# Optimization experiments

Measured on AMD Instinct MI355X. Metric: run time of the kernel, lower is better.

The kernel has to match this reference:

```python
import jax, jax.numpy as jnp
import numpy as np

B, T, D, H, OUT, VOCAB = 64, 100, 1024, 1024, 28, 28


def setup_inputs() -> dict:
    key = jax.random.key(0)
    ks = jax.random.split(key, 12)
    s = 0.05
    return {
        "x": jax.random.normal(ks[0], (B, T, D), jnp.float32),
        # encoder GRU (keras reset_after=True): kernel [D,3H], recurrent [H,3H], bias [2,3H]
        "enc_W": jax.random.normal(ks[1], (D, 3 * H), jnp.float32) * s,
        "enc_U": jax.random.normal(ks[2], (H, 3 * H), jnp.float32) * s,
        "enc_b": jax.random.normal(ks[3], (2, 3 * H), jnp.float32) * s,
        # AdditiveAttention learned scale vector [H]
        "att_scale": jax.random.normal(ks[4], (H,), jnp.float32) * s,
        # Embedding(28, H)
        "emb_W": jax.random.normal(ks[5], (VOCAB, H), jnp.float32) * s,
        # decoder GRUCell
        "dec_W": jax.random.normal(ks[6], (H, 3 * H), jnp.float32) * s,
        "dec_U": jax.random.normal(ks[7], (H, 3 * H), jnp.float32) * s,
        "dec_b": jax.random.normal(ks[8], (2, 3 * H), jnp.float32) * s,
        # fc: Dense(OUT) on concat([h, context]) -> [2H, OUT]
        "fc_W": jax.random.normal(ks[9], (2 * H, OUT), jnp.float32) * s,
        "fc_b": jax.random.normal(ks[10], (OUT,), jnp.float32) * s,
    }


def _gru_update(x_t, h, W, U, b):
    # keras GRU math with reset_after=True
    mx = x_t @ W + b[0]          # [B,3H]
    mi = h @ U + b[1]            # [B,3H]
    xz, xr, xh = jnp.split(mx, 3, axis=-1)
    rz, rr, rh = jnp.split(mi, 3, axis=-1)
    z = jax.nn.sigmoid(xz + rz)
    r = jax.nn.sigmoid(xr + rr)
    hh = jnp.tanh(xh + r * rh)
    return z * h + (1.0 - z) * hh


def reference(x, enc_W, enc_U, enc_b, att_scale, emb_W, dec_W, dec_U, dec_b, fc_W, fc_b):
    b, t, _ = x.shape
    h = jnp.zeros((b, enc_U.shape[0]), x.dtype)

    # encoder GRU, return_sequences=True
    def enc_step(h, x_t):
        h = _gru_update(x_t, h, enc_W, enc_U, enc_b)
        return h, h

    _, hpe = jax.lax.scan(enc_step, h, jnp.swapaxes(x, 0, 1))  # [T,B,H]
    hpe = jnp.swapaxes(hpe, 0, 1)                              # [B,T,H]

    out_dim = fc_b.shape[0]
    p0 = jnp.zeros((b, out_dim), x.dtype)
    h0 = jnp.zeros((b, dec_U.shape[0]), x.dtype)

    def dec_step(carry, _):
        p, hd = carry
        # additive attention: scores[b,j] = sum_d scale[d]*tanh(q[b,d]+k[b,j,d])
        scores = jnp.einsum('bth,h->bt', jnp.tanh(hd[:, None, :] + hpe), att_scale)
        attn = jax.nn.softmax(scores, axis=-1)
        ctx = jnp.einsum('bt,bth->bh', attn, hpe)
        idx = jnp.argmax(p, axis=-1)          # [B] int
        e = emb_W[idx]                        # [B,H]
        hd = _gru_update(e, hd, dec_W, dec_U, dec_b)
        p = jnp.concatenate([hd, ctx], axis=1) @ fc_W + fc_b
        return (p, hd), p

    _, outs = jax.lax.scan(dec_step, (p0, h0), None, length=t)  # [T,B,OUT]
    return jnp.swapaxes(outs, 0, 1)                              # [B,T,OUT]
```

## Files before the change

kernel.cpp:

```cpp
#include <hip/hip_runtime.h>

#define TT 100
#define HH 1024
#define H3 3072
#define NOUT 28

#define AGENT __HIP_MEMORY_SCOPE_AGENT
#define WGRP  __HIP_MEMORY_SCOPE_WORKGROUP
#define SPIN_CAP (1u<<27)

__device__ __forceinline__ float frcp_(float x){ return __builtin_amdgcn_rcpf(x); }
__device__ __forceinline__ float fsig_(float x){ return frcp_(1.0f + __expf(-x)); }
__device__ __forceinline__ float ftanh_(float x){ return 1.0f - 2.0f*frcp_(__expf(2.0f*x) + 1.0f); }

__device__ __forceinline__ unsigned long long aload8(const unsigned long long* p){
    return __hip_atomic_load(p, __ATOMIC_RELAXED, AGENT);
}
__device__ __forceinline__ unsigned aload4(const int* p){
    return (unsigned)__hip_atomic_load(p, __ATOMIC_RELAXED, AGENT);
}

__device__ __forceinline__ void gridbar(int* slot, int sub, int target){
    __syncthreads();
    if (threadIdx.x == 0){
        __hip_atomic_fetch_add(slot + sub*16, 1, __ATOMIC_RELAXED, AGENT);
        unsigned gy = 0; int s;
        do {
            s = 0;
            #pragma unroll
            for (int c=0;c<16;c++) s += __hip_atomic_load(slot + c*16, __ATOMIC_RELAXED, AGENT);
            if (s < target){ if (++gy > SPIN_CAP) break; __builtin_amdgcn_s_sleep(1); }
        } while (s < target);
    }
    __syncthreads();
}

__device__ __forceinline__ void wbar4(int* c, int tgt){
    asm volatile("s_waitcnt lgkmcnt(0)" ::: "memory");
    if ((threadIdx.x & 63) == 0) __hip_atomic_fetch_add(c, 1, __ATOMIC_RELAXED, WGRP);
    unsigned gy = 0;
    while (__hip_atomic_load(c, __ATOMIC_RELAXED, WGRP) < tgt){ if (++gy > SPIN_CAP) break; }
    asm volatile("" ::: "memory");
}

__global__ void k_init(int* ib, int n){
    int g = blockIdx.x*256 + threadIdx.x;
    if (g < n) ib[g] = 0;
}

__global__ __launch_bounds__(256) void k_transpose(const float* __restrict__ U0,
                                                   const float* __restrict__ U1,
                                                   float* __restrict__ T0,
                                                   float* __restrict__ T1){
    const float* U = blockIdx.z ? U1 : U0;
    float*       T = blockIdx.z ? T1 : T0;
    __shared__ float tile[32][33];
    int tx = threadIdx.x & 31, ty = threadIdx.x >> 5;
    int j0 = blockIdx.x*32, k0 = blockIdx.y*32;
    #pragma unroll
    for (int q=0;q<4;q++){
        int kr = ty + q*8;
        tile[kr][tx] = U[(size_t)(k0+kr)*H3 + j0 + tx];
    }
    __syncthreads();
    #pragma unroll
    for (int q=0;q<4;q++){
        int jr = ty + q*8;
        T[(size_t)(j0+jr)*HH + k0 + tx] = tile[tx][jr];
    }
}

__global__ __launch_bounds__(256) void k_edec(const float* __restrict__ emb,
                                              const float* __restrict__ W,
                                              const float* __restrict__ b0,
                                              float* __restrict__ E){
    int gid = blockIdx.x*256 + threadIdx.x;
    int v = gid / H3, j = gid - v*H3;
    float acc = b0[j];
    const float* er = emb + (size_t)v*HH;
    #pragma unroll 4
    for (int k=0;k<HH;k++) acc = fmaf(er[k], W[(size_t)k*H3 + j], acc);
    E[gid] = acc;
}

__global__ __launch_bounds__(256) void k_mxgemm(const float* __restrict__ A,
                                                const float* __restrict__ W,
                                                const float* __restrict__ b0,
                                                float* __restrict__ MXT){
    __shared__ float aT[32*68];
    __shared__ float bL[32*68];
    int tid = threadIdx.x;
    int row0 = blockIdx.y*64, col0 = blockIdx.x*64;
    int arow = tid>>2, acs = (tid&3)*4;
    int bk   = tid>>3, bcs = (tid&7)*4;
    int ty = tid>>4, tx = tid&15;
    float acc[4][4] = {};
    for (int kk=0; kk<HH; kk+=32){
        #pragma unroll
        for (int i=0;i<2;i++){
            int c = acs + i*16;
            float4 v = *(const float4*)(A + (size_t)(row0+arow)*HH + kk + c);
            aT[(c+0)*68 + arow] = v.x; aT[(c+1)*68 + arow] = v.y;
            aT[(c+2)*68 + arow] = v.z; aT[(c+3)*68 + arow] = v.w;
        }
        #pragma unroll
        for (int i=0;i<2;i++){
            int c = bcs + i*32;
            float4 v = *(const float4*)(W + (size_t)(kk+bk)*H3 + col0 + c);
            *(float4*)(bL + bk*68 + c) = v;
        }
        __syncthreads();
        #pragma unroll
        for (int k=0;k<32;k++){
            float4 a4 = *(const float4*)(aT + k*68 + ty*4);
            float4 b4 = *(const float4*)(bL + k*68 + tx*4);
            acc[0][0]=fmaf(a4.x,b4.x,acc[0][0]); acc[0][1]=fmaf(a4.x,b4.y,acc[0][1]);
            acc[0][2]=fmaf(a4.x,b4.z,acc[0][2]); acc[0][3]=fmaf(a4.x,b4.w,acc[0][3]);
            acc[1][0]=fmaf(a4.y,b4.x,acc[1][0]); acc[1][1]=fmaf(a4.y,b4.y,acc[1][1]);
            acc[1][2]=fmaf(a4.y,b4.z,acc[1][2]); acc[1][3]=fmaf(a4.y,b4.w,acc[1][3]);
            acc[2][0]=fmaf(a4.z,b4.x,acc[2][0]); acc[2][1]=fmaf(a4.z,b4.y,acc[2][1]);
            acc[2][2]=fmaf(a4.z,b4.z,acc[2][2]); acc[2][3]=fmaf(a4.z,b4.w,acc[2][3]);
            acc[3][0]=fmaf(a4.w,b4.x,acc[3][0]); acc[3][1]=fmaf(a4.w,b4.y,acc[3][1]);
            acc[3][2]=fmaf(a4.w,b4.z,acc[3][2]); acc[3][3]=fmaf(a4.w,b4.w,acc[3][3]);
        }
        __syncthreads();
    }
    float4 bb = *(const float4*)(b0 + col0 + tx*4);
    #pragma unroll
    for (int i=0;i<4;i++){
        int r = row0 + ty*4 + i;
        int bq = r / 100; int tq = r - bq*100;
        float v0 = acc[i][0] + bb.x, v1 = acc[i][1] + bb.y;
        float v2 = acc[i][2] + bb.z, v3 = acc[i][3] + bb.w;
        float* dst = MXT + ((size_t)tq*H3 + col0 + tx*4)*64 + bq;
        dst[0]   = v0; dst[64]  = v1; dst[128] = v2; dst[192] = v3;
    }
}

__global__ __launch_bounds__(256) void k_enc(const float* __restrict__ MXT,
                                             const float* __restrict__ Ut,
                                             const float* __restrict__ b1,
                                             float* __restrict__ hpe,
                                             float* __restrict__ hT,
                                             int* __restrict__ bar){
    __shared__ float hs[2][16384];
    int tid = threadIdx.x, lane = tid & 63;
    int wg = blockIdx.x;
    int sub = wg & 15;
    int cu = __builtin_amdgcn_readfirstlane(wg*4 + (tid>>6));
    const float* Uz = Ut + (size_t)cu*HH;
    const float* Ur = Uz + (size_t)HH*HH;
    const float* Uh = Ur + (size_t)HH*HH;
    float bz = b1[cu], br = b1[cu+HH], bh = b1[cu+2*HH];
    for (int t=0; t<TT; ++t){
        int cur = t & 1;
        const float* mx = MXT + (size_t)t*H3*64;
        float xz = mx[(size_t)cu*64 + lane];
        float xr = mx[(size_t)(cu+HH)*64 + lane];
        float xh = mx[(size_t)(cu+2*HH)*64 + lane];
        float az=0.f, ar=0.f, ah=0.f, hp=0.f;
        if (t > 0){
            const unsigned long long* g8 = (const unsigned long long*)(hT + (size_t)cur*65536);
            unsigned long long sv[32];
            #pragma unroll
            for (int s=0;s<32;s++) sv[s] = aload8(g8 + s*256 + tid);
            #pragma unroll
            for (int s=0;s<32;s++) ((unsigned long long*)hs[0])[s*256 + tid] = sv[s];
            __syncthreads();
            for (int q=0;q<4;++q){
                if (q<3){
                    #pragma unroll
                    for (int s=0;s<32;s++) sv[s] = aload8(g8 + (q+1)*8192 + s*256 + tid);
                }
                const float* hb = hs[q&1];
                const float* Uzq = Uz + q*256;
                const float* Urq = Ur + q*256;
                const float* Uhq = Uh + q*256;
                #pragma unroll 8
                for (int k=0;k<256;++k){
                    float h = hb[k*64 + lane];
                    az = fmaf(h, Uzq[k], az);
                    ar = fmaf(h, Urq[k], ar);
                    ah = fmaf(h, Uhq[k], ah);
                }
                if ((cu>>8) == q) hp = hb[(cu&255)*64 + lane];
                if (q<3){
                    #pragma unroll
                    for (int s=0;s<32;s++) ((unsigned long long*)hs[(q+1)&1])[s*256 + tid] = sv[s];
                }
                __syncthreads();
            }
        }
        float z  = fsig_(xz + az + bz);
        float r  = fsig_(xr + ar + br);
        float hh = ftanh_(xh + r*(ah + bh));
        float hnew = z*hp + (1.f - z)*hh;
        __hip_atomic_store(hT + (size_t)(cur^1)*65536 + cu*64 + lane, hnew, __ATOMIC_RELAXED, AGENT);
        hpe[((size_t)lane*TT + t)*HH + cu] = hnew;
        gridbar(bar + (size_t)t*256, sub, 256);
    }
}

__global__ __launch_bounds__(512) void k_dec(const float* __restrict__ hpe,
                                             const float* __restrict__ Ut,
                                             const float* __restrict__ b1,
                                             const float* __restrict__ Edec,
                                             const float* __restrict__ scale,
                                             const float* __restrict__ fcW,
                                             const float* __restrict__ fcb,
                                             float* __restrict__ hdT,
                                             float* __restrict__ hdl,
                                             float* __restrict__ out,
                                             int* __restrict__ idx_t,
                                             int* __restrict__ bar,
                                             int* __restrict__ flagidx){
    __shared__ float hs[2][16384];
    __shared__ float ctxs[4][1024];
    __shared__ float s_l[128], s_e[128], m_s[4], S_s[4];
    __shared__ int c_a, c_b, c_fc, go, cstg;
    int tid = threadIdx.x, wg = blockIdx.x;
    if (tid == 0){ c_a=0; c_b=0; c_fc=0; go=0; cstg=0; }
    __syncthreads();

    if (tid < 256){
        int lane = tid & 63;
        int sub = wg & 15;
        int cu = __builtin_amdgcn_readfirstlane(wg*4 + (tid>>6));
        const float* Uz = Ut + (size_t)cu*HH;
        const float* Ur = Uz + (size_t)HH*HH;
        const float* Uh = Ur + (size_t)HH*HH;
        float bz = b1[cu], br = b1[cu+HH], bh = b1[cu+2*HH];
        int stgt = 0;
        for (int i=0; i<TT; ++i){
            int cur = i & 1;
            float az=0.f, ar=0.f, ah=0.f, hp=0.f;
            if (i > 0){
                const unsigned long long* g8 = (const unsigned long long*)(hdT + (size_t)cur*65536);
                unsigned long long sv[32];
                #pragma unroll
                for (int s=0;s<32;s++) sv[s] = aload8(g8 + s*256 + tid);
                #pragma unroll
                for (int s=0;s<32;s++) ((unsigned long long*)hs[0])[s*256 + tid] = sv[s];
                wbar4(&cstg, stgt += 4);
                for (int q=0;q<4;++q){
                    if (q<3){
                        #pragma unroll
                        for (int s=0;s<32;s++) sv[s] = aload8(g8 + (q+1)*8192 + s*256 + tid);
                    }
                    const float* hb = hs[q&1];
                    const float* Uzq = Uz + q*256;
                    const float* Urq = Ur + q*256;
                    const float* Uhq = Uh + q*256;
                    #pragma unroll 8
                    for (int k=0;k<256;++k){
                        float h = hb[k*64 + lane];
                        az = fmaf(h, Uzq[k], az);
                        ar = fmaf(h, Urq[k], ar);
                        ah = fmaf(h, Uhq[k], ah);
                    }
                    if ((cu>>8) == q) hp = hb[(cu&255)*64 + lane];
                    if (q<3){
                        #pragma unroll
                        for (int s=0;s<32;s++) ((unsigned long long*)hs[(q+1)&1])[s*256 + tid] = sv[s];
                    }
                    wbar4(&cstg, stgt += 4);
                }
            }
            if (tid == 0){
                unsigned gy = 0; int s;
                do {
                    s = 0;
                    #pragma unroll
                    for (int c=0;c<8;c++) s += __hip_atomic_load(flagidx + (size_t)i*128 + c*16, __ATOMIC_RELAXED, AGENT);
                    if (s < 64){ if (++gy > SPIN_CAP) break; __builtin_amdgcn_s_sleep(1); }
                } while (s < 64);
                __hip_atomic_store(&go, i+1, __ATOMIC_RELAXED, WGRP);
            }
            { unsigned gy=0; while (__hip_atomic_load(&go, __ATOMIC_RELAXED, WGRP) < i+1){ if (++gy > SPIN_CAP) break; } }
            asm volatile("" ::: "memory");
            unsigned mi = aload4(idx_t + (size_t)i*64 + lane);
            if (mi > 27u) mi = 0;
            const float* ed = Edec + (size_t)mi*H3;
            float xz = ed[cu], xr = ed[cu+HH], xh = ed[cu+2*HH];
            float z  = fsig_(xz + az + bz);
            float r  = fsig_(xr + ar + br);
            float hh = ftanh_(xh + r*(ah + bh));
            float hnew = z*hp + (1.f - z)*hh;
            __hip_atomic_store(hdT + (size_t)(cur^1)*65536 + cu*64 + lane, hnew, __ATOMIC_RELAXED, AGENT);
            __hip_atomic_store(hdl + (size_t)(cur^1)*65536 + (size_t)lane*HH + cu, hnew, __ATOMIC_RELAXED, AGENT);
            gridbar(bar + (size_t)i*256, sub, 256);
        }
    } else if (wg < 64){
        int t2 = tid - 256;
        int w = t2 >> 6, lane = t2 & 63, b = wg;
        float sc[16];
        #pragma unroll
        for (int s4=0;s4<4;s4++){
            float4 v = *(const float4*)(scale + lane*16 + s4*4);
            sc[s4*4+0]=v.x; sc[s4*4+1]=v.y; sc[s4*4+2]=v.z; sc[s4*4+3]=v.w;
        }
        int j0 = w*25;
        for (int i=0; i<TT; ++i){
            float q[16];
            if (i == 0){
                #pragma unroll
                for (int d=0;d<16;d++) q[d]=0.f;
            } else {
                const unsigned long long* hq8 = (const unsigned long long*)(hdl + (size_t)(i&1)*65536 + (size_t)b*HH) + lane*8;
                #pragma unroll
                for (int s8=0;s8<8;s8++){
                    unsigned long long v = aload8(hq8 + s8);
                    q[2*s8+0] = __uint_as_float((unsigned)v);
                    q[2*s8+1] = __uint_as_float((unsigned)(v>>32));
                }
            }
            if (w == 0){
                if (i > 0){
                    float acc[NOUT];
                    #pragma unroll
                    for (int o=0;o<NOUT;o++) acc[o]=0.f;
                    float cv[16];
                    #pragma unroll
                    for (int s4=0;s4<4;s4++){
                        float4 c0 = ((const float4*)ctxs[0])[lane*4+s4];
                        float4 c1 = ((const float4*)ctxs[1])[lane*4+s4];
                        float4 c2 = ((const float4*)ctxs[2])[lane*4+s4];
                        float4 c3 = ((const float4*)ctxs[3])[lane*4+s4];
                        cv[s4*4+0]=c0.x+c1.x+c2.x+c3.x;
                        cv[s4*4+1]=c0.y+c1.y+c2.y+c3.y;
                        cv[s4*4+2]=c0.z+c1.z+c2.z+c3.z;
                        cv[s4*4+3]=c0.w+c1.w+c2.w+c3.w;
                    }
                    #pragma unroll
                    for (int dd=0;dd<16;++dd){
                        int d = lane*16 + dd;
                        const float* w0p = fcW + (size_t)d*NOUT;
                        const float* w1p = fcW + (size_t)(d+HH)*NOUT;
                        float hv=q[dd], cvv=cv[dd];
                        #pragma unroll
                        for (int o=0;o<NOUT;o++) acc[o] = fmaf(hv, w0p[o], fmaf(cvv, w1p[o], acc[o]));
                    }
                    #pragma unroll
                    for (int o=0;o<NOUT;o++){
                        #pragma unroll
                        for (int m=1;m<64;m<<=1) acc[o] += __shfl_xor(acc[o], m);
                    }
                    float bv=-3.0e38f; int bi=0;
                    #pragma unroll
                    for (int o=0;o<NOUT;o++){
                        float p = acc[o] + fcb[o];
                        acc[o] = p;
                        if (p > bv){ bv = p; bi = o; }
                    }
                    float vout = 0.f;
                    #pragma unroll
                    for (int o=0;o<NOUT;o++) if (lane == o) vout = acc[o];
                    if (lane < NOUT) out[((size_t)b*TT + (i-1))*NOUT + lane] = vout;
                    if (lane == 0){
                        __hip_atomic_store(idx_t + (size_t)i*64 + b, bi, __ATOMIC_RELAXED, AGENT);
                        asm volatile("s_waitcnt vmcnt(0)" ::: "memory");
                    }
                }
                if (lane == 0){
                    __hip_atomic_fetch_add(flagidx + (size_t)i*128 + (b&7)*16, 1, __ATOMIC_RELAXED, AGENT);
                    __hip_atomic_fetch_add(&c_fc, 1, __ATOMIC_RELAXED, WGRP);
                }
            }
            float mw = -3.0e38f;
            for (int jj=0;jj<25;jj++){
                int j = j0 + jj;
                const float* hpj = hpe + ((size_t)b*TT + j)*HH + lane*16;
                float s = 0.f;
                #pragma unroll
                for (int s4=0;s4<4;s4++){
                    float4 v = *(const float4*)(hpj + s4*4);
                    s += sc[s4*4+0]*ftanh_(q[s4*4+0] + v.x);
                    s += sc[s4*4+1]*ftanh_(q[s4*4+1] + v.y);
                    s += sc[s4*4+2]*ftanh_(q[s4*4+2] + v.z);
                    s += sc[s4*4+3]*ftanh_(q[s4*4+3] + v.w);
                }
                #pragma unroll
                for (int m=1;m<64;m<<=1) s += __shfl_xor(s, m);
                if (lane == 0) s_l[j] = s;
                mw = fmaxf(mw, s);
            }
            if (lane == 0) m_s[w] = mw;
            asm volatile("s_waitcnt lgkmcnt(0)" ::: "memory");
            if (lane == 0) __hip_atomic_fetch_add(&c_a, 1, __ATOMIC_RELAXED, WGRP);
            { unsigned gy=0; while (__hip_atomic_load(&c_a, __ATOMIC_RELAXED, WGRP) < 4*(i+1)){ if (++gy > SPIN_CAP) break; } }
            asm volatile("" ::: "memory");
            float M = fmaxf(fmaxf(m_s[0],m_s[1]), fmaxf(m_s[2],m_s[3]));
            float e = 0.f;
            if (lane < 25){ e = __expf(s_l[j0+lane] - M); s_e[j0+lane] = e; }
            float Sw = e;
            #pragma unroll
            for (int m=1;m<64;m<<=1) Sw += __shfl_xor(Sw, m);
            if (lane == 0) S_s[w] = Sw;
            asm volatile("s_waitcnt lgkmcnt(0)" ::: "memory");
            if (lane == 0) __hip_atomic_fetch_add(&c_b, 1, __ATOMIC_RELAXED, WGRP);
            { unsigned gy=0; while (__hip_atomic_load(&c_b, __ATOMIC_RELAXED, WGRP) < 4*(i+1)){ if (++gy > SPIN_CAP) break; } }
            asm volatile("" ::: "memory");
            float rinv = frcp_(S_s[0]+S_s[1]+S_s[2]+S_s[3]);
            { unsigned gy=0; while (__hip_atomic_load(&c_fc, __ATOMIC_RELAXED, WGRP) < i+1){ if (++gy > SPIN_CAP) break; } }
            asm volatile("" ::: "memory");
            float a[16];
            #pragma unroll
            for (int s4=0;s4<16;s4++) a[s4]=0.f;
            for (int jj=0;jj<25;jj++){
                int j = j0 + jj;
                float wgt = s_e[j];
                const float* hpj = hpe + ((size_t)b*TT + j)*HH + lane*16;
                #pragma unroll
                for (int s4=0;s4<4;s4++){
                    float4 v = *(const float4*)(hpj + s4*4);
                    a[s4*4+0] = fmaf(wgt, v.x, a[s4*4+0]);
                    a[s4*4+1] = fmaf(wgt, v.y, a[s4*4+1]);
                    a[s4*4+2] = fmaf(wgt, v.z, a[s4*4+2]);
                    a[s4*4+3] = fmaf(wgt, v.w, a[s4*4+3]);
                }
            }
            #pragma unroll
            for (int s4=0;s4<4;s4++){
                float4 o4;
                o4.x=a[s4*4+0]*rinv; o4.y=a[s4*4+1]*rinv;
                o4.z=a[s4*4+2]*rinv; o4.w=a[s4*4+3]*rinv;
                ((float4*)ctxs[w])[lane*4 + s4] = o4;
            }
            gridbar(bar + (size_t)i*256, wg & 15, 256);
        }
        if (w == 0){
            const unsigned long long* hq8 = (const unsigned long long*)(hdl + (size_t)b*HH) + lane*8;
            float q[16];
            #pragma unroll
            for (int s8=0;s8<8;s8++){
                unsigned long long v = aload8(hq8 + s8);
                q[2*s8+0] = __uint_as_float((unsigned)v);
                q[2*s8+1] = __uint_as_float((unsigned)(v>>32));
            }
            float acc[NOUT];
            #pragma unroll
            for (int o=0;o<NOUT;o++) acc[o]=0.f;
            float cv[16];
            #pragma unroll
            for (int s4=0;s4<4;s4++){
                float4 c0 = ((const float4*)ctxs[0])[lane*4+s4];
                float4 c1 = ((const float4*)ctxs[1])[lane*4+s4];
                float4 c2 = ((const float4*)ctxs[2])[lane*4+s4];
                float4 c3 = ((const float4*)ctxs[3])[lane*4+s4];
                cv[s4*4+0]=c0.x+c1.x+c2.x+c3.x;
                cv[s4*4+1]=c0.y+c1.y+c2.y+c3.y;
                cv[s4*4+2]=c0.z+c1.z+c2.z+c3.z;
                cv[s4*4+3]=c0.w+c1.w+c2.w+c3.w;
            }
            #pragma unroll
            for (int dd=0;dd<16;++dd){
                int d = lane*16 + dd;
                const float* w0p = fcW + (size_t)d*NOUT;
                const float* w1p = fcW + (size_t)(d+HH)*NOUT;
                float hv=q[dd], cvv=cv[dd];
                #pragma unroll
                for (int o=0;o<NOUT;o++) acc[o] = fmaf(hv, w0p[o], fmaf(cvv, w1p[o], acc[o]));
            }
            #pragma unroll
            for (int o=0;o<NOUT;o++){
                #pragma unroll
                for (int m=1;m<64;m<<=1) acc[o] += __shfl_xor(acc[o], m);
            }
            float vout = 0.f;
            #pragma unroll
            for (int o=0;o<NOUT;o++) if (lane == o) vout = acc[o] + fcb[o];
            if (lane < NOUT) out[((size_t)b*TT + 99)*NOUT + lane] = vout;
        }
    } else {
        for (int i=0;i<TT;++i) gridbar(bar + (size_t)i*256, wg & 15, 256);
    }
}

extern "C" void kernel_launch(void* const* d_in, const int* in_sizes, int n_in,
                              void* d_out, int out_size, void* d_ws, size_t ws_size,
                              hipStream_t stream){
    (void)in_sizes; (void)n_in; (void)out_size; (void)ws_size;
    const float* x     = (const float*)d_in[0];
    const float* encW  = (const float*)d_in[1];
    const float* encU  = (const float*)d_in[2];
    const float* encb  = (const float*)d_in[3];
    const float* scale = (const float*)d_in[4];
    const float* emb   = (const float*)d_in[5];
    const float* decW  = (const float*)d_in[6];
    const float* decU  = (const float*)d_in[7];
    const float* decb  = (const float*)d_in[8];
    const float* fcW   = (const float*)d_in[9];
    const float* fcb   = (const float*)d_in[10];
    float* out = (float*)d_out;
    float* ws  = (float*)d_ws;

    float* MXT   = ws;
    float* encUt = MXT   + 19660800;
    float* decUt = encUt + 3145728;
    float* hpe   = decUt + 3145728;
    float* Edec  = hpe   + 6553600;
    float* hT    = Edec  + 86016;
    float* hdT   = hT    + 131072;
    float* hdl   = hdT   + 131072;
    int*   ib    = (int*)(hdl + 131072);
    int*   bar_enc = ib;
    int*   bar_dec = ib + 25600;
    int*   flagidx = ib + 51200;
    int*   idx_t   = ib + 64000;

    const float* encb1 = encb + H3;
    const float* decb1 = decb + H3;

    k_init<<<276,256,0,stream>>>(ib, 70400);
    k_transpose<<<dim3(96,32,2),256,0,stream>>>(encU, decU, encUt, decUt);
    k_edec<<<336,256,0,stream>>>(emb, decW, decb, Edec);
    k_mxgemm<<<dim3(48,100),256,0,stream>>>(x, encW, encb, MXT);
    k_enc<<<256,256,0,stream>>>(MXT, encUt, encb1, hpe, hT, bar_enc);
    k_dec<<<256,512,0,stream>>>(hpe, decUt, decb1, Edec, scale, fcW, fcb,
                                hdT, hdl, out, idx_t, bar_dec, flagidx);
}
```

Measured before the change: 11.06 ms.

## Fuse attention scores, softmax and context into single online-softmax pass

The decoder attention now computes scores, a running max/sum and the weighted context accumulation in one pass over hpe per wave, using online-softmax rescaling. This removes the second read of hpe and one intra-workgroup sync stage. The four wave partials are merged by rescaling against the global max. It also lowers the spin cap and aliases the decoder state buffers onto the dead MXT workspace. The cost is extra exp and rescale multiplies per timestep.

```diff
diff --git a/kernel.cpp b/kernel.cpp
--- a/kernel.cpp
+++ b/kernel.cpp
@@ -7,7 +7,7 @@
 
 #define AGENT __HIP_MEMORY_SCOPE_AGENT
 #define WGRP  __HIP_MEMORY_SCOPE_WORKGROUP
-#define SPIN_CAP (1u<<27)
+#define SPIN_CAP (1u<<20)
 
 __device__ __forceinline__ float frcp_(float x){ return __builtin_amdgcn_rcpf(x); }
 __device__ __forceinline__ float fsig_(float x){ return frcp_(1.0f + __expf(-x)); }
@@ -216,10 +216,10 @@
                                              int* __restrict__ flagidx){
     __shared__ float hs[2][16384];
     __shared__ float ctxs[4][1024];
-    __shared__ float s_l[128], s_e[128], m_s[4], S_s[4];
-    __shared__ int c_a, c_b, c_fc, go, cstg;
+    __shared__ float m_s[4], S_s[4];
+    __shared__ int c_a, c_fc, go, cstg;
     int tid = threadIdx.x, wg = blockIdx.x;
-    if (tid == 0){ c_a=0; c_b=0; c_fc=0; go=0; cstg=0; }
+    if (tid == 0){ c_a=0; c_fc=0; go=0; cstg=0; }
     __syncthreads();
 
     if (tid < 256){
@@ -366,64 +366,53 @@
                     __hip_atomic_fetch_add(&c_fc, 1, __ATOMIC_RELAXED, WGRP);
                 }
             }
-            float mw = -3.0e38f;
+            float m = -3.0e38f, S = 0.f;
+            float a[16];
+            #pragma unroll
+            for (int d=0;d<16;d++) a[d]=0.f;
             for (int jj=0;jj<25;jj++){
                 int j = j0 + jj;
                 const float* hpj = hpe + ((size_t)b*TT + j)*HH + lane*16;
+                float va[16];
+                {
+                    float4 v0 = *(const float4*)(hpj);
+                    float4 v1 = *(const float4*)(hpj+4);
+                    float4 v2 = *(const float4*)(hpj+8);
+                    float4 v3 = *(const float4*)(hpj+12);
+                    va[0]=v0.x;va[1]=v0.y;va[2]=v0.z;va[3]=v0.w;
+                    va[4]=v1.x;va[5]=v1.y;va[6]=v1.z;va[7]=v1.w;
+                    va[8]=v2.x;va[9]=v2.y;va[10]=v2.z;va[11]=v2.w;
+                    va[12]=v3.x;va[13]=v3.y;va[14]=v3.z;va[15]=v3.w;
+                }
                 float s = 0.f;
                 #pragma unroll
-                for (int s4=0;s4<4;s4++){
-                    float4 v = *(const float4*)(hpj + s4*4);
-                    s += sc[s4*4+0]*ftanh_(q[s4*4+0] + v.x);
-                    s += sc[s4*4+1]*ftanh_(q[s4*4+1] + v.y);
-                    s += sc[s4*4+2]*ftanh_(q[s4*4+2] + v.z);
-                    s += sc[s4*4+3]*ftanh_(q[s4*4+3] + v.w);
-                }
-                #pragma unroll
-                for (int m=1;m<64;m<<=1) s += __shfl_xor(s, m);
-                if (lane == 0) s_l[j] = s;
-                mw = fmaxf(mw, s);
-            }
-            if (lane == 0) m_s[w] = mw;
+                for (int d=0;d<16;d++) s += sc[d]*ftanh_(q[d] + va[d]);
+                #pragma unroll
+                for (int mm=1;mm<64;mm<<=1) s += __shfl_xor(s, mm);
+                float mn = fmaxf(m, s);
+                float fold = __expf(m - mn);
+                float e = __expf(s - mn);
+                S = S*fold + e;
+                #pragma unroll
+                for (int d=0;d<16;d++) a[d] = a[d]*fold + e*va[d];
+                m = mn;
+            }
+            if (lane == 0){ m_s[w] = m; S_s[w] = S; }
             asm volatile("s_waitcnt lgkmcnt(0)" ::: "memory");
             if (lane == 0) __hip_atomic_fetch_add(&c_a, 1, __ATOMIC_RELAXED, WGRP);
             { unsigned gy=0; while (__hip_atomic_load(&c_a, __ATOMIC_RELAXED, WGRP) < 4*(i+1)){ if (++gy > SPIN_CAP) break; } }
             asm volatile("" ::: "memory");
             float M = fmaxf(fmaxf(m_s[0],m_s[1]), fmaxf(m_s[2],m_s[3]));
-            float e = 0.f;
-            if (lane < 25){ e = __expf(s_l[j0+lane] - M); s_e[j0+lane] = e; }
-            float Sw = e;
-            #pragma unroll
-            for (int m=1;m<64;m<<=1) Sw += __shfl_xor(Sw, m);
-            if (lane == 0) S_s[w] = Sw;
-            asm volatile("s_waitcnt lgkmcnt(0)" ::: "memory");
-            if (lane == 0) __hip_atomic_fetch_add(&c_b, 1, __ATOMIC_RELAXED, WGRP);
-            { unsigned gy=0; while (__hip_atomic_load(&c_b, __ATOMIC_RELAXED, WGRP) < 4*(i+1)){ if (++gy > SPIN_CAP) break; } }
-            asm volatile("" ::: "memory");
-            float rinv = frcp_(S_s[0]+S_s[1]+S_s[2]+S_s[3]);
+            float St = S_s[0]*__expf(m_s[0]-M) + S_s[1]*__expf(m_s[1]-M)
+                     + S_s[2]*__expf(m_s[2]-M) + S_s[3]*__expf(m_s[3]-M);
+            float g = __expf(m - M) * frcp_(St);
             { unsigned gy=0; while (__hip_atomic_load(&c_fc, __ATOMIC_RELAXED, WGRP) < i+1){ if (++gy > SPIN_CAP) break; } }
             asm volatile("" ::: "memory");
-            float a[16];
-            #pragma unroll
-            for (int s4=0;s4<16;s4++) a[s4]=0.f;
-            for (int jj=0;jj<25;jj++){
-                int j = j0 + jj;
-                float wgt = s_e[j];
-                const float* hpj = hpe + ((size_t)b*TT + j)*HH + lane*16;
-                #pragma unroll
-                for (int s4=0;s4<4;s4++){
-                    float4 v = *(const float4*)(hpj + s4*4);
-                    a[s4*4+0] = fmaf(wgt, v.x, a[s4*4+0]);
-                    a[s4*4+1] = fmaf(wgt, v.y, a[s4*4+1]);
-                    a[s4*4+2] = fmaf(wgt, v.z, a[s4*4+2]);
-                    a[s4*4+3] = fmaf(wgt, v.w, a[s4*4+3]);
-                }
-            }
             #pragma unroll
             for (int s4=0;s4<4;s4++){
                 float4 o4;
-                o4.x=a[s4*4+0]*rinv; o4.y=a[s4*4+1]*rinv;
-                o4.z=a[s4*4+2]*rinv; o4.w=a[s4*4+3]*rinv;
+                o4.x=a[s4*4+0]*g; o4.y=a[s4*4+1]*g;
+                o4.z=a[s4*4+2]*g; o4.w=a[s4*4+3]*g;
                 ((float4*)ctxs[w])[lane*4 + s4] = o4;
             }
             gridbar(bar + (size_t)i*256, wg & 15, 256);
@@ -495,14 +484,14 @@
     float* ws  = (float*)d_ws;
 
     float* MXT   = ws;
+    float* hdT   = MXT;
+    float* hdl   = MXT + 131072;
     float* encUt = MXT   + 19660800;
     float* decUt = encUt + 3145728;
     float* hpe   = decUt + 3145728;
     float* Edec  = hpe   + 6553600;
     float* hT    = Edec  + 86016;
-    float* hdT   = hT    + 131072;
-    float* hdl   = hdT   + 131072;
-    int*   ib    = (int*)(hdl + 131072);
+    int*   ib    = (int*)(hT + 131072);
     int*   bar_enc = ib;
     int*   bar_dec = ib + 25600;
     int*   flagidx = ib + 51200;
```

New measurement: 10.90 ms. Within noise of the previous version (-1.5%).
